# Kernel optimization log

Hardware: AMD Instinct MI355X
Metric: run time of the kernel (lower is better)

Reference implementation:

```python
import jax, jax.numpy as jnp
import numpy as np

N_NODES = 50000
N_EDGES = 800000
N_GRAPHS = 256
FEAT = 128
HID = 64
HEADS = 4
OUT = 128
NEG_SLOPE = 0.2  # PyG GATConv default leaky_relu slope


def setup_inputs() -> dict:
    key = jax.random.key(0)
    ks = jax.random.split(key, 16)
    x = jax.random.normal(ks[0], (N_NODES, FEAT), dtype=jnp.float32)
    edge_index = jax.random.randint(ks[1], (2, N_EDGES), 0, N_NODES, dtype=jnp.int64)
    batch = jnp.sort(jax.random.randint(ks[2], (N_NODES,), 0, N_GRAPHS, dtype=jnp.int64))
    dims_in = [FEAT, HID * HEADS, HID * HEADS]
    params = {}
    for i, din in enumerate(dims_in):
        s = 1.0 / np.sqrt(din)
        params[f"W{i}"] = jax.random.normal(ks[3 + 4 * i], (din, HEADS * HID), dtype=jnp.float32) * s
        params[f"as{i}"] = jax.random.normal(ks[4 + 4 * i], (HEADS, HID), dtype=jnp.float32) * s
        params[f"ad{i}"] = jax.random.normal(ks[5 + 4 * i], (HEADS, HID), dtype=jnp.float32) * s
        params[f"b{i}"] = jnp.zeros((HEADS * HID,), dtype=jnp.float32)
    params["Wf"] = jax.random.normal(ks[15], (HID * HEADS, OUT), dtype=jnp.float32) / np.sqrt(HID * HEADS)
    params["bf"] = jnp.zeros((OUT,), dtype=jnp.float32)
    return {"x": x, "edge_index": edge_index, "batch": batch, **params}


def _gat_layer(x, src, dst, W, a_s, a_d, b):
    # x: [N, Din] -> h: [N, H, D]
    N = x.shape[0]
    h = (x @ W).reshape(N, HEADS, HID)
    alpha_src = jnp.einsum("nhd,hd->nh", h, a_s)  # [N, H]
    alpha_dst = jnp.einsum("nhd,hd->nh", h, a_d)
    e = jax.nn.leaky_relu(alpha_src[src] + alpha_dst[dst], NEG_SLOPE)  # [E, H]
    # segment softmax over edges sharing the same destination node
    m = jax.ops.segment_max(e, dst, num_segments=N)
    ex = jnp.exp(e - m[dst])
    s = jax.ops.segment_sum(ex, dst, num_segments=N)
    alpha = ex / s[dst]  # [E, H]
    msg = h[src] * alpha[:, :, None]  # [E, H, D]
    out = jax.ops.segment_sum(msg, dst, num_segments=N)  # [N, H, D]
    return out.reshape(N, HEADS * HID) + b


def reference(x, edge_index, batch, W0, as0, ad0, b0, W1, as1, ad1, b1,
              W2, as2, ad2, b2, Wf, bf):
    N = x.shape[0]
    loop = jnp.arange(N, dtype=edge_index.dtype)
    src = jnp.concatenate([edge_index[0], loop])  # PyG GATConv adds self-loops
    dst = jnp.concatenate([edge_index[1], loop])
    for W, a_s, a_d, b in ((W0, as0, ad0, b0), (W1, as1, ad1, b1), (W2, as2, ad2, b2)):
        x = jax.nn.elu(_gat_layer(x, src, dst, W, a_s, a_d, b))
    # global mean pool over graphs
    sums = jax.ops.segment_sum(x, batch, num_segments=N_GRAPHS)  # [G, HID*HEADS]
    cnt = jax.ops.segment_sum(jnp.ones((N,), x.dtype), batch, num_segments=N_GRAPHS)
    g = sums / jnp.maximum(cnt, 1.0)[:, None]
    y = g @ Wf + bf
    norm = jnp.linalg.norm(y, axis=-1, keepdims=True)
    return y / jnp.maximum(norm, 1e-12)
```

## Files before the change

### kernel.cpp

```cpp
#include <hip/hip_runtime.h>
#include <math.h>

#define NND 50000
#define NED 800000
#define ETOT 850000
#define NG 256
#define FEAT 128
#define CCH 256
#define OUTD 128
#define NEG 0.2f
#define NBLK 196
#define M2 50048
#define XBLK 6250

typedef __attribute__((ext_vector_type(8))) _Float16 half8;
typedef __attribute__((ext_vector_type(4))) _Float16 half4;
typedef __attribute__((ext_vector_type(4))) float floatx4;

#if __has_builtin(__builtin_amdgcn_global_load_lds)
#define GLOAD16(g, l) __builtin_amdgcn_global_load_lds( \
    (const __attribute__((address_space(1))) void*)(g), \
    (__attribute__((address_space(3))) void*)(l), 16, 0, 0)
#define HAVE_GLDS 1
#else
#define HAVE_GLDS 0
#endif


__global__ void count_kernel(const int* __restrict__ ei, int* __restrict__ deg) {
    int e = blockIdx.x * 256 + threadIdx.x;
    if (e >= ETOT) return;
    int dst = (e < NED) ? ei[NED + e] : (e - NED);
    atomicAdd(&deg[dst], 1);
}

__global__ __launch_bounds__(256) void scan_part_kernel(const int* __restrict__ deg,
                                                        int* __restrict__ bsum) {
    __shared__ int tile[256];
    int i = blockIdx.x * 256 + threadIdx.x;
    tile[threadIdx.x] = (i < NND) ? deg[i] : 0;
    __syncthreads();
    for (int s = 128; s > 0; s >>= 1) {
        if (threadIdx.x < s) tile[threadIdx.x] += tile[threadIdx.x + s];
        __syncthreads();
    }
    if (threadIdx.x == 0) bsum[blockIdx.x] = tile[0];
}

__global__ __launch_bounds__(256) void scan_write_kernel(const int* __restrict__ deg,
                                                         const int* __restrict__ bsum,
                                                         int* __restrict__ rowptr,
                                                         int* __restrict__ cursor) {
    __shared__ int bs[256];
    __shared__ int tile[256];
    const int t = threadIdx.x, b = blockIdx.x;
    bs[t] = (t < NBLK) ? bsum[t] : 0;
    __syncthreads();
    for (int off = 1; off < 256; off <<= 1) {
        int u = (t >= off) ? bs[t - off] : 0;
        __syncthreads();
        bs[t] += u;
        __syncthreads();
    }
    int boffb = (b == 0) ? 0 : bs[b - 1];
    int total = bs[NBLK - 1];
    int i = b * 256 + t;
    int v = (i < NND) ? deg[i] : 0;
    tile[t] = v;
    __syncthreads();
    for (int off = 1; off < 256; off <<= 1) {
        int u = (t >= off) ? tile[t - off] : 0;
        __syncthreads();
        tile[t] += u;
        __syncthreads();
    }
    if (i < NND) {
        int r = boffb + tile[t] - v;
        rowptr[i] = r;
        cursor[i] = r;
    }
    if (i == 0) rowptr[NND] = total;
}

__global__ void scatter_kernel(const int* __restrict__ ei, int* __restrict__ cursor,
                               int* __restrict__ csrsrc) {
    int e = blockIdx.x * 256 + threadIdx.x;
    if (e >= ETOT) return;
    int s, d;
    if (e < NED) { s = ei[e]; d = ei[NED + e]; } else { s = d = e - NED; }
    int pos = atomicAdd(&cursor[d], 1);
    csrsrc[pos] = s;
}


__global__ __launch_bounds__(256) void prep_kernel(const int* __restrict__ batch,
                                                   int* __restrict__ deg,
                                                   int* __restrict__ gstart,
                                                   const float4* __restrict__ x,
                                                   half4* __restrict__ xo,
                                                   const float* __restrict__ W0,
                                                   const float* __restrict__ W1,
                                                   const float* __restrict__ W2,
                                                   _Float16* __restrict__ wt0,
                                                   _Float16* __restrict__ wt1,
                                                   _Float16* __restrict__ wt2) {
    int b = blockIdx.x;
    if (b < 196) {
        int i = b * 256 + threadIdx.x;
        if (i < NND + 1) deg[i] = 0;
        return;
    }
    b -= 196;
    if (b < 196) {
        int i = b * 256 + threadIdx.x;
        if (i >= NND) return;
        int bb = batch[i];
        int bp = (i == 0) ? -1 : batch[i - 1];
        for (int g = bp + 1; g <= bb; ++g) gstart[g] = i;
        if (i == NND - 1)
            for (int g = bb + 1; g <= NG; ++g) gstart[g] = NND;
        return;
    }
    b -= 196;
    if (b < XBLK) {
        int i = b * 256 + threadIdx.x;
        if (i >= NND * FEAT / 4) return;
        float4 v = x[i];
        half4 o;
        o[0] = (_Float16)v.x; o[1] = (_Float16)v.y;
        o[2] = (_Float16)v.z; o[3] = (_Float16)v.w;
        xo[i] = o;
        return;
    }
    b -= XBLK;
    int j = b * 256 + threadIdx.x;
    if (j < 256 * 128) {
        int n = j >> 7, k = j & 127;
        wt0[j] = (_Float16)W0[k * 256 + n];
        return;
    }
    j -= 256 * 128;
    if (j < 256 * 256) {
        int n = j >> 8, k = j & 255;
        wt1[j] = (_Float16)W1[k * 256 + n];
        return;
    }
    j -= 256 * 256;
    if (j < 256 * 256) {
        int n = j >> 8, k = j & 255;
        wt2[j] = (_Float16)W2[k * 256 + n];
    }
}


#define BK 64

__global__ __launch_bounds__(256, 3) void gemm_mfma_kernel(
        const _Float16* __restrict__ A,
        const _Float16* __restrict__ Bt,
        const float* __restrict__ as_, const float* __restrict__ ad_,
        _Float16* __restrict__ Hm,
        float* __restrict__ asrc, float* __restrict__ adst, int K) {
    __shared__ _Float16 AsF[64 * 64];
    __shared__ _Float16 BsF[256 * 64];
    const int t = threadIdx.x;
    const int bm = blockIdx.x * 64;
    const int lane = t & 63, wv = t >> 6;
    const int wn = wv * 64;
    const int fr = lane & 15, q = lane >> 4;

    floatx4 acc[4][4] = {};

    const int lrow = t >> 3;
    const int c8 = t & 7;

    for (int k0 = 0; k0 < K; k0 += BK) {
        for (int p = 0; p < 2; p++) {
            int row = p * 32 + lrow;
            int g8 = c8 ^ (row & 7);
            const _Float16* ga = A + (size_t)(bm + row) * K + k0 + g8 * 8;
#if HAVE_GLDS
            GLOAD16(ga, &AsF[row * 64 + c8 * 8]);
#else
            *(half8*)&AsF[row * 64 + c8 * 8] = *(const half8*)ga;
#endif
        }
        for (int p = 0; p < 8; p++) {
            int row = p * 32 + lrow;
            int g8 = c8 ^ (row & 7);
            const _Float16* gb = Bt + (size_t)row * K + k0 + g8 * 8;
#if HAVE_GLDS
            GLOAD16(gb, &BsF[row * 64 + c8 * 8]);
#else
            *(half8*)&BsF[row * 64 + c8 * 8] = *(const half8*)gb;
#endif
        }
        __syncthreads();
        for (int kc = 0; kc < 2; kc++) {
            half8 af[4], bf[4];
            int kb = kc * 4 + q;
            int cs = (kb ^ (fr & 7)) * 8;
            for (int mi = 0; mi < 4; mi++)
                af[mi] = *(const half8*)&AsF[(mi * 16 + fr) * 64 + cs];
            for (int ni = 0; ni < 4; ni++)
                bf[ni] = *(const half8*)&BsF[(wn + ni * 16 + fr) * 64 + cs];
            for (int mi = 0; mi < 4; mi++)
                for (int ni = 0; ni < 4; ni++)
                    acc[mi][ni] = __builtin_amdgcn_mfma_f32_16x16x32_f16(
                        af[mi], bf[ni], acc[mi][ni], 0, 0, 0);
        }
        __syncthreads();
    }

    for (int mi = 0; mi < 4; mi++) {
        int row0 = bm + mi * 16 + q * 4;
        for (int ni = 0; ni < 4; ni++) {
            int col = wn + ni * 16 + fr;
            for (int r = 0; r < 4; r++)
                Hm[(size_t)(row0 + r) * CCH + col] = (_Float16)acc[mi][ni][r];
        }
    }

    const int hd = wv;
    float asf[4], adf[4];
    for (int ni = 0; ni < 4; ni++) {
        asf[ni] = as_[hd * 64 + ni * 16 + fr];
        adf[ni] = ad_[hd * 64 + ni * 16 + fr];
    }
    for (int mi = 0; mi < 4; mi++)
        for (int r = 0; r < 4; r++) {
            float ps = 0.f, pd = 0.f;
            for (int ni = 0; ni < 4; ni++) {
                float v = acc[mi][ni][r];
                ps += v * asf[ni];
                pd += v * adf[ni];
            }
            for (int m = 1; m < 16; m <<= 1) {
                ps += __shfl_xor(ps, m, 64);
                pd += __shfl_xor(pd, m, 64);
            }
            if (fr == 0) {
                int row = bm + mi * 16 + q * 4 + r;
                asrc[row * 4 + hd] = ps;
                adst[row * 4 + hd] = pd;
            }
        }
}


__global__ __launch_bounds__(256) void agg_kernel(const _Float16* __restrict__ H16,
                                                  const float* __restrict__ asrc,
                                                  const float* __restrict__ adst,
                                                  const int* __restrict__ rowptr,
                                                  const int* __restrict__ csrsrc,
                                                  const float4* __restrict__ bias4,
                                                  half8* __restrict__ xo) {
    int wave = threadIdx.x >> 6, lane = threadIdx.x & 63;
    int n = blockIdx.x * 4 + wave;
    if (n >= NND) return;
    int rs = rowptr[n], re = rowptr[n + 1];
    int hd = lane >> 4;
    int sub = lane & 15;
    int l32 = lane & 31;
    int myh = l32 >> 3;
    int epar = lane >> 5;
    float adv = adst[n * 4 + hd];
    float acc[8] = {};
    float ssum = 0.f;
    const char* hbyte = (const char*)H16;
    unsigned loff = (unsigned)l32 * 16u;

    int sl = rs + sub;
    bool ok = sl < re;
    int idx = ok ? csrsrc[sl] : 0;
    unsigned off = (unsigned)idx << 9;
    float aval = asrc[idx * 4 + hd];

    int e0 = rs;
    while (re - e0 >= 16) {
        float a = aval + adv;
        a = fmaxf(a, NEG * a);
        float ev = __expf(a);
        ssum += ev;
        unsigned offcur = off;
        int sl2 = e0 + 16 + sub;
        bool ok2 = sl2 < re;
        int idx2 = ok2 ? csrsrc[sl2] : 0;
        off = (unsigned)idx2 << 9;
        aval = asrc[idx2 * 4 + hd];
        ok = ok2;

        half8 hv[8];
        float wws[8];
        #pragma unroll
        for (int j2 = 0; j2 < 8; j2++) {
            int j = j2 * 2 + epar;
            unsigned o = __shfl(offcur, j, 64);
            wws[j2] = __shfl(ev, myh * 16 + j, 64);
            hv[j2] = *(const half8*)(hbyte + (o + loff));
        }
        #pragma unroll
        for (int j2 = 0; j2 < 8; j2++) {
            float ww = wws[j2];
            #pragma unroll
            for (int k = 0; k < 8; k++)
                acc[k] += ww * (float)hv[j2][k];
        }
        e0 += 16;
    }
    if (e0 < re) {
        float a = aval + adv;
        a = fmaxf(a, NEG * a);
        float ev = ok ? __expf(a) : 0.f;
        ssum += ev;
        int cnt = re - e0;
        #pragma unroll
        for (int j2 = 0; j2 < 8; j2++) {
            if (j2 * 2 >= cnt) break;
            int j = j2 * 2 + epar;
            unsigned o = __shfl(off, j, 64);
            float ww = __shfl(ev, myh * 16 + j, 64);
            half8 hv = *(const half8*)(hbyte + (o + loff));
            #pragma unroll
            for (int k = 0; k < 8; k++)
                acc[k] += ww * (float)hv[k];
        }
    }
    for (int sft = 1; sft < 16; sft <<= 1) ssum += __shfl_xor(ssum, sft, 64);
    float inv = 1.f / __shfl(ssum, myh * 16, 64);
    #pragma unroll
    for (int k = 0; k < 8; k++) acc[k] += __shfl_xor(acc[k], 32, 64);
    if (lane < 32) {
        float4 b0 = bias4[l32 * 2], b1 = bias4[l32 * 2 + 1];
        float o[8];
        o[0] = acc[0] * inv + b0.x; o[1] = acc[1] * inv + b0.y;
        o[2] = acc[2] * inv + b0.z; o[3] = acc[3] * inv + b0.w;
        o[4] = acc[4] * inv + b1.x; o[5] = acc[5] * inv + b1.y;
        o[6] = acc[6] * inv + b1.z; o[7] = acc[7] * inv + b1.w;
        half8 h;
        #pragma unroll
        for (int k = 0; k < 8; k++) {
            float v = o[k];
            v = v > 0.f ? v : expm1f(v);
            h[k] = (_Float16)v;
        }
        xo[(size_t)n * 32 + l32] = h;
    }
}


__global__ __launch_bounds__(1024) void poolfinal_kernel(const _Float16* __restrict__ xa,
                                                         const int* __restrict__ gstart,
                                                         const float* __restrict__ Wf,
                                                         const float* __restrict__ bfv,
                                                         float* __restrict__ out) {
    int g = blockIdx.x, t = threadIdx.x;
    int ch = t & 255, qt = t >> 8;
    __shared__ float part[4][256];
    __shared__ float gm[256];
    __shared__ float mm[8][128];
    __shared__ float red[128];
    int s = gstart[g], e = gstart[g + 1];
    int cnt = e - s;
    float acc = 0.f;
    for (int i = s + qt; i < e; i += 4)
        acc += (float)xa[(size_t)i * CCH + ch];
    part[qt][ch] = acc;
    __syncthreads();
    if (qt == 0)
        gm[ch] = (part[0][ch] + part[1][ch] + part[2][ch] + part[3][ch])
                 / (float)(cnt > 0 ? cnt : 1);
    __syncthreads();
    int j = t & 127, ks = t >> 7;
    float a = 0.f;
    for (int k = ks * 32; k < ks * 32 + 32; k++)
        a += gm[k] * Wf[k * OUTD + j];
    mm[ks][j] = a;
    __syncthreads();
    if (t < OUTD) {
        float v = bfv[j];
        for (int q = 0; q < 8; q++) v += mm[q][j];
        red[j] = v * v;
        mm[0][j] = v;
    }
    __syncthreads();
    for (int sft = 64; sft > 0; sft >>= 1) {
        if (t < sft) red[t] += red[t + sft];
        __syncthreads();
    }
    if (t < OUTD) out[g * OUTD + t] = mm[0][t] / fmaxf(sqrtf(red[0]), 1e-12f);
}


extern "C" void kernel_launch(void* const* d_in, const int* in_sizes, int n_in,
                              void* d_out, int out_size, void* d_ws, size_t ws_size,
                              hipStream_t stream) {
    const float* x     = (const float*)d_in[0];
    const int*   ei    = (const int*)d_in[1];
    const int*   batch = (const int*)d_in[2];
    const float* W[3]  = {(const float*)d_in[3], (const float*)d_in[7],  (const float*)d_in[11]};
    const float* As[3] = {(const float*)d_in[4], (const float*)d_in[8],  (const float*)d_in[12]};
    const float* Ad[3] = {(const float*)d_in[5], (const float*)d_in[9],  (const float*)d_in[13]};
    const float* Bb[3] = {(const float*)d_in[6], (const float*)d_in[10], (const float*)d_in[14]};
    const float* Wf    = (const float*)d_in[15];
    const float* bf    = (const float*)d_in[16];
    float* out = (float*)d_out;

    _Float16* H16   = (_Float16*)d_ws;
    _Float16* act16 = H16 + (size_t)M2 * CCH;
    _Float16* wt0   = act16 + (size_t)M2 * CCH;
    _Float16* wt1   = wt0 + 256 * 128;
    _Float16* wt2   = wt1 + 256 * 256;
    float* asrc  = (float*)(wt2 + 256 * 256);
    float* adst  = asrc + (size_t)M2 * 4;
    int* deg     = (int*)(adst + (size_t)M2 * 4);
    int* rowptr  = deg + (NND + 1);
    int* cursor  = rowptr + (NND + 1);
    int* csrsrc  = cursor + (NND + 1);
    int* gstart  = csrsrc + ETOT;
    int* bsum    = gstart + (NG + 1);

    _Float16* wt[3] = {wt0, wt1, wt2};

    prep_kernel<<<196 + 196 + XBLK + 640, 256, 0, stream>>>(
        batch, deg, gstart, (const float4*)x, (half4*)act16,
        W[0], W[1], W[2], wt0, wt1, wt2);
    count_kernel<<<(ETOT + 255) / 256, 256, 0, stream>>>(ei, deg);
    scan_part_kernel<<<NBLK, 256, 0, stream>>>(deg, bsum);
    scan_write_kernel<<<NBLK, 256, 0, stream>>>(deg, bsum, rowptr, cursor);
    scatter_kernel<<<(ETOT + 255) / 256, 256, 0, stream>>>(ei, cursor, csrsrc);

    int K = FEAT;
    for (int l = 0; l < 3; l++) {
        gemm_mfma_kernel<<<M2 / 64, 256, 0, stream>>>(act16, wt[l], As[l], Ad[l], H16, asrc, adst, K);
        agg_kernel<<<(NND + 3) / 4, 256, 0, stream>>>(H16, asrc, adst, rowptr, csrsrc,
                                                      (const float4*)Bb[l], (half8*)act16);
        K = CCH;
    }

    poolfinal_kernel<<<NG, 1024, 0, stream>>>(act16, gstart, Wf, bf, out);
}
```

Measured before the change: 479.2 us.

## Fold degree counting into prep and CSR scatter into first GEMM launch

Degree counting now runs as extra blocks of the prep kernel, with deg zeroed by a memset instead of prep blocks. The CSR scatter runs as extra blocks appended to the layer-0 GEMM grid, which also lets it overlap with that GEMM. This drops two kernel launches and their serialization. The extra scatter blocks still need the 65KB of static LDS that the GEMM kernel declares, which may limit how many can be resident. The count blocks in prep may run at the same time as the other prep work.

```diff
diff --git a/kernel.cpp b/kernel.cpp
--- a/kernel.cpp
+++ b/kernel.cpp
@@ -12,6 +12,8 @@
 #define NBLK 196
 #define M2 50048
 #define XBLK 6250
+#define SCATBLK 3321
+#define GEMMBLK (M2 / 64)
 
 typedef __attribute__((ext_vector_type(8))) _Float16 half8;
 typedef __attribute__((ext_vector_type(4))) _Float16 half4;
@@ -27,13 +29,6 @@
 #endif
 
 
-__global__ void count_kernel(const int* __restrict__ ei, int* __restrict__ deg) {
-    int e = blockIdx.x * 256 + threadIdx.x;
-    if (e >= ETOT) return;
-    int dst = (e < NED) ? ei[NED + e] : (e - NED);
-    atomicAdd(&deg[dst], 1);
-}
-
 __global__ __launch_bounds__(256) void scan_part_kernel(const int* __restrict__ deg,
                                                         int* __restrict__ bsum) {
     __shared__ int tile[256];
@@ -80,16 +75,6 @@
         cursor[i] = r;
     }
     if (i == 0) rowptr[NND] = total;
-}
-
-__global__ void scatter_kernel(const int* __restrict__ ei, int* __restrict__ cursor,
-                               int* __restrict__ csrsrc) {
-    int e = blockIdx.x * 256 + threadIdx.x;
-    if (e >= ETOT) return;
-    int s, d;
-    if (e < NED) { s = ei[e]; d = ei[NED + e]; } else { s = d = e - NED; }
-    int pos = atomicAdd(&cursor[d], 1);
-    csrsrc[pos] = s;
 }
 
 
@@ -103,14 +88,9 @@
                                                    const float* __restrict__ W2,
                                                    _Float16* __restrict__ wt0,
                                                    _Float16* __restrict__ wt1,
-                                                   _Float16* __restrict__ wt2) {
+                                                   _Float16* __restrict__ wt2,
+                                                   const int* __restrict__ ei) {
     int b = blockIdx.x;
-    if (b < 196) {
-        int i = b * 256 + threadIdx.x;
-        if (i < NND + 1) deg[i] = 0;
-        return;
-    }
-    b -= 196;
     if (b < 196) {
         int i = b * 256 + threadIdx.x;
         if (i >= NND) return;
@@ -149,6 +129,12 @@
     if (j < 256 * 256) {
         int n = j >> 8, k = j & 255;
         wt2[j] = (_Float16)W2[k * 256 + n];
+        return;
+    }
+    j -= 256 * 256;
+    if (j < ETOT) {
+        int dst = (j < NED) ? ei[NED + j] : (j - NED);
+        atomicAdd(&deg[dst], 1);
     }
 }
 
@@ -160,7 +146,20 @@
         const _Float16* __restrict__ Bt,
         const float* __restrict__ as_, const float* __restrict__ ad_,
         _Float16* __restrict__ Hm,
-        float* __restrict__ asrc, float* __restrict__ adst, int K) {
+        float* __restrict__ asrc, float* __restrict__ adst, int K,
+        int gemmBlocks,
+        const int* __restrict__ ei, int* __restrict__ cursor,
+        int* __restrict__ csrsrc) {
+    if ((int)blockIdx.x >= gemmBlocks) {
+        int e = ((int)blockIdx.x - gemmBlocks) * 256 + threadIdx.x;
+        if (e < ETOT) {
+            int s, d;
+            if (e < NED) { s = ei[e]; d = ei[NED + e]; } else { s = d = e - NED; }
+            int pos = atomicAdd(&cursor[d], 1);
+            csrsrc[pos] = s;
+        }
+        return;
+    }
     __shared__ _Float16 AsF[64 * 64];
     __shared__ _Float16 BsF[256 * 64];
     const int t = threadIdx.x;
@@ -422,17 +421,20 @@
 
     _Float16* wt[3] = {wt0, wt1, wt2};
 
-    prep_kernel<<<196 + 196 + XBLK + 640, 256, 0, stream>>>(
+    hipMemsetAsync(deg, 0, (NND + 1) * sizeof(int), stream);
+
+    prep_kernel<<<196 + XBLK + 640 + SCATBLK, 256, 0, stream>>>(
         batch, deg, gstart, (const float4*)x, (half4*)act16,
-        W[0], W[1], W[2], wt0, wt1, wt2);
-    count_kernel<<<(ETOT + 255) / 256, 256, 0, stream>>>(ei, deg);
+        W[0], W[1], W[2], wt0, wt1, wt2, ei);
     scan_part_kernel<<<NBLK, 256, 0, stream>>>(deg, bsum);
     scan_write_kernel<<<NBLK, 256, 0, stream>>>(deg, bsum, rowptr, cursor);
-    scatter_kernel<<<(ETOT + 255) / 256, 256, 0, stream>>>(ei, cursor, csrsrc);
 
     int K = FEAT;
     for (int l = 0; l < 3; l++) {
-        gemm_mfma_kernel<<<M2 / 64, 256, 0, stream>>>(act16, wt[l], As[l], Ad[l], H16, asrc, adst, K);
+        int grid = (l == 0) ? (GEMMBLK + SCATBLK) : GEMMBLK;
+        gemm_mfma_kernel<<<grid, 256, 0, stream>>>(act16, wt[l], As[l], Ad[l], H16,
+                                                   asrc, adst, K, GEMMBLK,
+                                                   ei, cursor, csrsrc);
         agg_kernel<<<(NND + 3) / 4, 256, 0, stream>>>(H16, asrc, adst, rowptr, csrsrc,
                                                       (const float4*)Bb[l], (half8*)act16);
         K = CCH;
```

New measurement: 484.0 us. No clear change (+1.0%).
